# Performance work log

Measured on AMD Instinct MI355X. Metric: run time of the kernel, lower is better.

Reference implementation:

```python
import jax, jax.numpy as jnp
import numpy as np

B, IN, H = 8192, 1024, 1024


def setup_inputs() -> dict:
    key = jax.random.key(0)
    ks = jax.random.split(key, 12)
    s_in = 1.0 / np.sqrt(IN + H)  # torch Linear default init scale
    inp = {
        "x": jax.random.normal(ks[0], (B, IN), jnp.float32),
        "h_prev": jax.random.normal(ks[1], (B, H), jnp.float32),
        "c_prev": jax.random.normal(ks[2], (B, H), jnp.float32),
        "embed": jax.random.normal(ks[3], (B, H), jnp.float32),
    }
    for i, g in enumerate(("forget", "input", "update", "out")):
        inp[f"W_{g}"] = jax.random.uniform(ks[4 + 2 * i], (IN + H, H), jnp.float32, -s_in, s_in)
        inp[f"b_{g}"] = jax.random.uniform(ks[5 + 2 * i], (H,), jnp.float32, -s_in, s_in)
    return inp


def reference(x, h_prev, c_prev, embed,
              W_forget, b_forget, W_input, b_input,
              W_update, b_update, W_out, b_out):
    # cat_input: [B, IN+H]; embed is accepted but unused (matches source forward)
    cat_input = jnp.concatenate((x.reshape(x.shape[0], -1), h_prev), axis=1)
    # Fuse the 4 gate GEMMs into one [B, IN+H] x [IN+H, 4H] matmul (same math)
    W = jnp.concatenate((W_forget, W_input, W_update, W_out), axis=1)  # [IN+H, 4H]
    b = jnp.concatenate((b_forget, b_input, b_update, b_out))          # [4H]
    gates = cat_input @ W + b                                          # [B, 4H]
    f_t, i_t, g_t, o_t = jnp.split(gates, 4, axis=1)
    f_t = jax.nn.sigmoid(f_t)
    i_t = jax.nn.sigmoid(i_t)
    c_opt = jnp.tanh(g_t)
    c_t = c_prev * f_t + i_t * c_opt
    o_t = jax.nn.sigmoid(o_t)
    h_t = o_t * jnp.tanh(c_t)
    return (h_t, c_t)
```

## Files before the change

kernel.cpp:

```cpp
#include <hip/hip_runtime.h>
#include <hip/hip_bf16.h>


typedef __attribute__((ext_vector_type(8))) short short8;
typedef __attribute__((ext_vector_type(4))) float f32x4;

#define GLOBAL_AS __attribute__((address_space(1)))
#define LDS_AS    __attribute__((address_space(3)))

__device__ __forceinline__ void load_lds16(const void* g, void* l) {
  __builtin_amdgcn_global_load_lds((const GLOBAL_AS unsigned int*)g,
                                   (LDS_AS unsigned int*)l, 16, 0, 0);
}

__device__ __forceinline__ unsigned short f2bf(float f) {
  unsigned int u = __float_as_uint(f);
  unsigned int r = (u + 0x7FFFu + ((u >> 16) & 1u)) >> 16;
  return (unsigned short)r;
}

__device__ __forceinline__ float sigf(float x) {
  return 1.0f / (1.0f + __expf(-x));
}
__device__ __forceinline__ float tanh_fast(float x) {
  return 1.0f - 2.0f / (__expf(2.0f * x) + 1.0f);
}

__global__ void pack_a_kernel(const float* __restrict__ x,
                              const float* __restrict__ h,
                              unsigned short* __restrict__ Apk) {
  int t = blockIdx.x * 256 + threadIdx.x;
  int row = t >> 8;
  int c   = t & 255;
  int k   = c << 3;
  const float* src = (k < 1024) ? (x + (size_t)row * 1024 + k)
                                : (h + (size_t)row * 1024 + (k - 1024));
  float4 f0 = ((const float4*)src)[0];
  float4 f1 = ((const float4*)src)[1];
  union { unsigned short us[8]; uint4 v; } u;
  u.us[0] = f2bf(f0.x); u.us[1] = f2bf(f0.y);
  u.us[2] = f2bf(f0.z); u.us[3] = f2bf(f0.w);
  u.us[4] = f2bf(f1.x); u.us[5] = f2bf(f1.y);
  u.us[6] = f2bf(f1.z); u.us[7] = f2bf(f1.w);
  int dc = (c & ~7) | ((c & 7) ^ (row & 7));
  *(uint4*)(Apk + (size_t)row * 2048 + dc * 8) = u.v;
}

__global__ void pack_w_kernel(const float* __restrict__ W0,
                              const float* __restrict__ W1,
                              const float* __restrict__ W2,
                              const float* __restrict__ W3,
                              unsigned short* __restrict__ Wp) {
  int b  = blockIdx.x;
  int c  = b & 255;
  int nb = (b >> 8) & 3;
  int g  = b >> 10;
  const float* Wg = (g == 0) ? W0 : (g == 1) ? W1 : (g == 2) ? W2 : W3;
  int np = nb * 256 + threadIdx.x;
  int kbase = c << 3;
  union { unsigned short us[8]; uint4 v; } u;
#pragma unroll
  for (int j = 0; j < 8; ++j)
    u.us[j] = f2bf(Wg[(size_t)(kbase + j) * 1024 + np]);
  int n = (g << 10) + np;
  int dc = (c & ~7) | ((c & 7) ^ (n & 7));
  *(uint4*)(Wp + (size_t)n * 2048 + dc * 8) = u.v;
}

__global__ __launch_bounds__(256) void lstm_gemm_kernel(
    const unsigned short* __restrict__ Apk,
    const unsigned short* __restrict__ Wp,
    const float* __restrict__ c_prev,
    const float* __restrict__ bF, const float* __restrict__ bI,
    const float* __restrict__ bU, const float* __restrict__ bO,
    float* __restrict__ outH, float* __restrict__ outC) {
  __shared__ __align__(16) unsigned short Abuf[128 * 64];
  __shared__ __align__(16) unsigned short Bbuf[128 * 64];

  const int tid = threadIdx.x;
  const int l   = tid & 63;
  const int w   = tid >> 6;
  const int wr  = w >> 1;
  const int wc  = w & 1;

  int bid = blockIdx.x;
  int wg  = ((bid & 7) << 8) | (bid >> 3);
  int mblk = wg >> 5;
  int nblk = wg & 31;
  int brow  = mblk << 7;
  int ncol0 = nblk << 5;

  f32x4 acc[4][4];
#pragma unroll
  for (int g = 0; g < 4; ++g)
#pragma unroll
    for (int m = 0; m < 4; ++m) acc[g][m] = (f32x4)0.0f;

  const int seg0  = w << 2;
  const int rlane = l >> 3;
  const int clane = l & 7;

  const unsigned short* agbase =
      Apk + (size_t)(brow + seg0 * 8 + rlane) * 2048 + clane * 8;

  for (int kt = 0; kt < 32; ++kt) {
    const int kofs = kt << 6;
#pragma unroll
    for (int i = 0; i < 4; ++i) {
      load_lds16(agbase + (size_t)i * 8 * 2048 + kofs, &Abuf[(seg0 + i) * 512]);
    }
#pragma unroll
    for (int i = 0; i < 4; ++i) {
      int j = (seg0 + i) * 8 + rlane;
      int grow = ((j >> 5) << 10) + ncol0 + (j & 31);
      load_lds16(Wp + (size_t)grow * 2048 + kofs + clane * 8,
                 &Bbuf[(seg0 + i) * 512]);
    }
    __syncthreads();

#pragma unroll
    for (int kk = 0; kk < 2; ++kk) {
      const int ck = (kk << 2) | (l >> 4);
      const int sc = ck ^ (l & 7);
      short8 a[4], bfr[4];
#pragma unroll
      for (int m = 0; m < 4; ++m) {
        int row = wr * 64 + m * 16 + (l & 15);
        a[m] = *(const short8*)&Abuf[row * 64 + sc * 8];
      }
#pragma unroll
      for (int g = 0; g < 4; ++g) {
        int j = g * 32 + wc * 16 + (l & 15);
        bfr[g] = *(const short8*)&Bbuf[j * 64 + sc * 8];
      }
#pragma unroll
      for (int g = 0; g < 4; ++g)
#pragma unroll
        for (int m = 0; m < 4; ++m)
          acc[g][m] = __builtin_amdgcn_mfma_f32_16x16x32_bf16(
              a[m], bfr[g], acc[g][m], 0, 0, 0);
    }
    __syncthreads();
  }

  const int colh = ncol0 + wc * 16 + (l & 15);
  const float biasF = bF[colh], biasI = bI[colh];
  const float biasU = bU[colh], biasO = bO[colh];
  const int rowbase = brow + wr * 64 + ((l >> 4) << 2);
#pragma unroll
  for (int m = 0; m < 4; ++m) {
#pragma unroll
    for (int r = 0; r < 4; ++r) {
      int row = rowbase + m * 16 + r;
      size_t idx = (size_t)row * 1024 + colh;
      float f  = sigf(acc[0][m][r] + biasF);
      float i_ = sigf(acc[1][m][r] + biasI);
      float g_ = tanh_fast(acc[2][m][r] + biasU);
      float o_ = sigf(acc[3][m][r] + biasO);
      float cp = c_prev[idx];
      float cn = cp * f + i_ * g_;
      outH[idx] = o_ * tanh_fast(cn);
      outC[idx] = cn;
    }
  }
}

extern "C" void kernel_launch(void* const* d_in, const int* in_sizes, int n_in,
                              void* d_out, int out_size, void* d_ws, size_t ws_size,
                              hipStream_t stream) {
  const float* x      = (const float*)d_in[0];
  const float* h_prev = (const float*)d_in[1];
  const float* c_prev = (const float*)d_in[2];
  const float* Wf = (const float*)d_in[4];
  const float* bf = (const float*)d_in[5];
  const float* Wi = (const float*)d_in[6];
  const float* bi = (const float*)d_in[7];
  const float* Wu = (const float*)d_in[8];
  const float* bu = (const float*)d_in[9];
  const float* Wo = (const float*)d_in[10];
  const float* bo = (const float*)d_in[11];

  unsigned short* Apk = (unsigned short*)d_ws;
  unsigned short* Wp  = (unsigned short*)((char*)d_ws + (size_t)8192 * 2048 * 2);

  pack_a_kernel<<<8192, 256, 0, stream>>>(x, h_prev, Apk);
  pack_w_kernel<<<4096, 256, 0, stream>>>(Wf, Wi, Wu, Wo, Wp);

  float* outH = (float*)d_out;
  float* outC = outH + (size_t)8192 * 1024;
  lstm_gemm_kernel<<<2048, 256, 0, stream>>>(Apk, Wp, c_prev,
                                             bf, bi, bu, bo, outH, outC);
}
```

Baseline: 201.1 us.

## Rewrite LSTM GEMM as 256x256-tile, 8-wave, 4-stage pipelined LDS kernel

The GEMM kernel now uses 256x256 output tiles (64 hidden columns across 4 gates) with 8 waves per block and 128 KB of dynamic LDS. The LDS is a 4-slot ring of 32-wide K chunks prefetched with global_load_lds, and waits are manual vmcnt counts plus raw s_barrier. MFMA phases are split per half-tile and raised with s_setprio so loads overlap compute. Global swizzling is dropped from the pack kernels and moved into the per-lane load address. The aim is more reuse per LDS byte and hiding memory latency, at the cost of higher register pressure, a single-block-per-CU LDS footprint, and fragile hand-written synchronization.

```diff
diff --git a/kernel.cpp b/kernel.cpp
--- a/kernel.cpp
+++ b/kernel.cpp
@@ -15,13 +15,9 @@
 
 __device__ __forceinline__ unsigned short f2bf(float f) {
   unsigned int u = __float_as_uint(f);
-  unsigned int r = (u + 0x7FFFu + ((u >> 16) & 1u)) >> 16;
-  return (unsigned short)r;
-}
-
-__device__ __forceinline__ float sigf(float x) {
-  return 1.0f / (1.0f + __expf(-x));
-}
+  return (unsigned short)((u + 0x7FFFu + ((u >> 16) & 1u)) >> 16);
+}
+__device__ __forceinline__ float sigf(float x) { return 1.0f / (1.0f + __expf(-x)); }
 __device__ __forceinline__ float tanh_fast(float x) {
   return 1.0f - 2.0f / (__expf(2.0f * x) + 1.0f);
 }
@@ -42,8 +38,7 @@
   u.us[2] = f2bf(f0.z); u.us[3] = f2bf(f0.w);
   u.us[4] = f2bf(f1.x); u.us[5] = f2bf(f1.y);
   u.us[6] = f2bf(f1.z); u.us[7] = f2bf(f1.w);
-  int dc = (c & ~7) | ((c & 7) ^ (row & 7));
-  *(uint4*)(Apk + (size_t)row * 2048 + dc * 8) = u.v;
+  *(uint4*)(Apk + (size_t)row * 2048 + c * 8) = u.v;
 }
 
 __global__ void pack_w_kernel(const float* __restrict__ W0,
@@ -63,100 +58,134 @@
   for (int j = 0; j < 8; ++j)
     u.us[j] = f2bf(Wg[(size_t)(kbase + j) * 1024 + np]);
   int n = (g << 10) + np;
-  int dc = (c & ~7) | ((c & 7) ^ (n & 7));
-  *(uint4*)(Wp + (size_t)n * 2048 + dc * 8) = u.v;
-}
-
-__global__ __launch_bounds__(256) void lstm_gemm_kernel(
+  *(uint4*)(Wp + (size_t)n * 2048 + c * 8) = u.v;
+}
+
+#define MFMA16(va, vb, vc) __builtin_amdgcn_mfma_f32_16x16x32_bf16(va, vb, vc, 0, 0, 0)
+
+#define PHASE(J, Q, KTP, PSLOT, WAITN)                                         \
+  {                                                                            \
+    const int slotUS = (J) * 8192;                                             \
+    short8 av[4];                                                              \
+    _Pragma("unroll")                                                          \
+    for (int mm = 0; mm < 4; ++mm)                                             \
+      av[mm] = *(const short8*)&LDSu[slotUS + aRdBase + ((Q) * 4 + mm) * 512]; \
+    if ((Q) == 0) {                                                            \
+      _Pragma("unroll")                                                        \
+      for (int gg = 0; gg < 4; ++gg)                                           \
+        bv[gg] = *(const short8*)&LDSu[32768 + slotUS + bRdBase + gg * 512];   \
+    }                                                                          \
+    int ktp = (KTP); ktp = (ktp > 31) ? 31 : ktp;                              \
+    const int srcOfs = ktp * 64 + ((PSLOT) & 1) * 32;                          \
+    const int pbase = (PSLOT) * 8192;                                          \
+    if ((Q) == 0) {                                                            \
+      load_lds16(aSrc0 + srcOfs, &LDSu[pbase + wv * 512]);                     \
+      load_lds16(aSrc1 + srcOfs, &LDSu[pbase + 4096 + wv * 512]);              \
+    } else {                                                                   \
+      load_lds16(bSrc0 + srcOfs, &LDSu[32768 + pbase + wv * 512]);             \
+      load_lds16(bSrc1 + srcOfs, &LDSu[32768 + pbase + 4096 + wv * 512]);      \
+    }                                                                          \
+    asm volatile("s_barrier" ::: "memory");                                    \
+    __builtin_amdgcn_s_setprio(1);                                             \
+    _Pragma("unroll")                                                          \
+    for (int mm = 0; mm < 4; ++mm) {                                           \
+      _Pragma("unroll")                                                        \
+      for (int gg = 0; gg < 4; ++gg)                                           \
+        acc[(Q) * 4 + mm][gg] = MFMA16(av[mm], bv[gg], acc[(Q) * 4 + mm][gg]); \
+    }                                                                          \
+    __builtin_amdgcn_s_setprio(0);                                             \
+    if ((WAITN) == 8) asm volatile("s_waitcnt vmcnt(8)" ::: "memory");         \
+    if ((WAITN) == 4) asm volatile("s_waitcnt vmcnt(4)" ::: "memory");         \
+    asm volatile("s_barrier" ::: "memory");                                    \
+  }
+
+__global__ __launch_bounds__(512, 2) void lstm_gemm_kernel(
     const unsigned short* __restrict__ Apk,
     const unsigned short* __restrict__ Wp,
     const float* __restrict__ c_prev,
     const float* __restrict__ bF, const float* __restrict__ bI,
     const float* __restrict__ bU, const float* __restrict__ bO,
     float* __restrict__ outH, float* __restrict__ outC) {
-  __shared__ __align__(16) unsigned short Abuf[128 * 64];
-  __shared__ __align__(16) unsigned short Bbuf[128 * 64];
+  extern __shared__ unsigned short LDSu[];
 
   const int tid = threadIdx.x;
   const int l   = tid & 63;
-  const int w   = tid >> 6;
-  const int wr  = w >> 1;
-  const int wc  = w & 1;
+  const int wv  = tid >> 6;
+  const int wr  = wv >> 2;
+  const int wc  = wv & 3;
 
   int bid = blockIdx.x;
-  int wg  = ((bid & 7) << 8) | (bid >> 3);
-  int mblk = wg >> 5;
-  int nblk = wg & 31;
-  int brow  = mblk << 7;
-  int ncol0 = nblk << 5;
-
-  f32x4 acc[4][4];
-#pragma unroll
-  for (int g = 0; g < 4; ++g)
-#pragma unroll
-    for (int m = 0; m < 4; ++m) acc[g][m] = (f32x4)0.0f;
-
-  const int seg0  = w << 2;
-  const int rlane = l >> 3;
-  const int clane = l & 7;
-
-  const unsigned short* agbase =
-      Apk + (size_t)(brow + seg0 * 8 + rlane) * 2048 + clane * 8;
-
-  for (int kt = 0; kt < 32; ++kt) {
-    const int kofs = kt << 6;
-#pragma unroll
-    for (int i = 0; i < 4; ++i) {
-      load_lds16(agbase + (size_t)i * 8 * 2048 + kofs, &Abuf[(seg0 + i) * 512]);
-    }
-#pragma unroll
-    for (int i = 0; i < 4; ++i) {
-      int j = (seg0 + i) * 8 + rlane;
-      int grow = ((j >> 5) << 10) + ncol0 + (j & 31);
-      load_lds16(Wp + (size_t)grow * 2048 + kofs + clane * 8,
-                 &Bbuf[(seg0 + i) * 512]);
-    }
-    __syncthreads();
-
-#pragma unroll
-    for (int kk = 0; kk < 2; ++kk) {
-      const int ck = (kk << 2) | (l >> 4);
-      const int sc = ck ^ (l & 7);
-      short8 a[4], bfr[4];
-#pragma unroll
-      for (int m = 0; m < 4; ++m) {
-        int row = wr * 64 + m * 16 + (l & 15);
-        a[m] = *(const short8*)&Abuf[row * 64 + sc * 8];
-      }
-#pragma unroll
-      for (int g = 0; g < 4; ++g) {
-        int j = g * 32 + wc * 16 + (l & 15);
-        bfr[g] = *(const short8*)&Bbuf[j * 64 + sc * 8];
-      }
-#pragma unroll
-      for (int g = 0; g < 4; ++g)
-#pragma unroll
-        for (int m = 0; m < 4; ++m)
-          acc[g][m] = __builtin_amdgcn_mfma_f32_16x16x32_bf16(
-              a[m], bfr[g], acc[g][m], 0, 0, 0);
-    }
-    __syncthreads();
+  int wg  = ((bid & 7) << 6) | (bid >> 3);
+  const int mblk = wg >> 4;
+  const int nblk = wg & 15;
+  const int brow = mblk << 8;
+
+  const int rl  = l & 15;
+  const int cg  = l >> 4;
+  const int sc  = cg ^ ((rl >> 1) & 3);
+  const int aRdBase = (wr * 128 + rl) * 32 + sc * 8;
+  const int bRdBase = (wc * 64 + rl) * 32 + sc * 8;
+
+  const int srow = wv * 16 + (l >> 2);
+  const int csw  = ((l & 3) ^ ((l >> 3) & 3)) * 8;
+  const unsigned short* aSrc0 = Apk + (size_t)(brow + srow) * 2048 + csw;
+  const unsigned short* aSrc1 = aSrc0 + (size_t)128 * 2048;
+  int p0 = nblk * 256 + srow;
+  int n0 = (((p0 >> 4) & 3) << 10) | ((p0 >> 6) << 4) | (p0 & 15);
+  int p1 = p0 + 128;
+  int n1 = (((p1 >> 4) & 3) << 10) | ((p1 >> 6) << 4) | (p1 & 15);
+  const unsigned short* bSrc0 = Wp + (size_t)n0 * 2048 + csw;
+  const unsigned short* bSrc1 = Wp + (size_t)n1 * 2048 + csw;
+
+  f32x4 acc[8][4];
+#pragma unroll
+  for (int m = 0; m < 8; ++m)
+#pragma unroll
+    for (int g = 0; g < 4; ++g) acc[m][g] = (f32x4)0.0f;
+
+  load_lds16(aSrc0 + 0,  &LDSu[0 + wv * 512]);
+  load_lds16(aSrc1 + 0,  &LDSu[4096 + wv * 512]);
+  load_lds16(bSrc0 + 0,  &LDSu[32768 + wv * 512]);
+  load_lds16(bSrc1 + 0,  &LDSu[32768 + 4096 + wv * 512]);
+  load_lds16(aSrc0 + 32, &LDSu[8192 + wv * 512]);
+  load_lds16(aSrc1 + 32, &LDSu[8192 + 4096 + wv * 512]);
+  load_lds16(bSrc0 + 32, &LDSu[32768 + 8192 + wv * 512]);
+  load_lds16(bSrc1 + 32, &LDSu[32768 + 8192 + 4096 + wv * 512]);
+  load_lds16(aSrc0 + 64, &LDSu[16384 + wv * 512]);
+  load_lds16(aSrc1 + 64, &LDSu[16384 + 4096 + wv * 512]);
+  load_lds16(bSrc0 + 64, &LDSu[32768 + 16384 + wv * 512]);
+  load_lds16(bSrc1 + 64, &LDSu[32768 + 16384 + 4096 + wv * 512]);
+  asm volatile("s_waitcnt vmcnt(4)" ::: "memory");
+  asm volatile("s_barrier" ::: "memory");
+
+#pragma unroll 1
+  for (int it = 0; it < 16; ++it) {
+    const int k2 = it << 1;
+    short8 bv[4];
+    PHASE(0, 0, k2 + 1, 3, -1)
+    PHASE(0, 1, k2 + 1, 3, -1)
+    PHASE(1, 0, k2 + 2, 0, -1)
+    PHASE(1, 1, k2 + 2, 0, 8)
+    PHASE(2, 0, k2 + 2, 1, -1)
+    PHASE(2, 1, k2 + 2, 1, 8)
+    PHASE(3, 0, k2 + 3, 2, -1)
+    PHASE(3, 1, k2 + 3, 2, 4)
   }
 
-  const int colh = ncol0 + wc * 16 + (l & 15);
+  const int colh = nblk * 64 + wc * 16 + rl;
   const float biasF = bF[colh], biasI = bI[colh];
   const float biasU = bU[colh], biasO = bO[colh];
-  const int rowbase = brow + wr * 64 + ((l >> 4) << 2);
-#pragma unroll
-  for (int m = 0; m < 4; ++m) {
+  const int row0 = brow + wr * 128 + ((l >> 4) << 2);
+#pragma unroll
+  for (int m = 0; m < 8; ++m) {
 #pragma unroll
     for (int r = 0; r < 4; ++r) {
-      int row = rowbase + m * 16 + r;
+      int row = row0 + m * 16 + r;
       size_t idx = (size_t)row * 1024 + colh;
-      float f  = sigf(acc[0][m][r] + biasF);
-      float i_ = sigf(acc[1][m][r] + biasI);
-      float g_ = tanh_fast(acc[2][m][r] + biasU);
-      float o_ = sigf(acc[3][m][r] + biasO);
+      float f  = sigf(acc[m][0][r] + biasF);
+      float i_ = sigf(acc[m][1][r] + biasI);
+      float g_ = tanh_fast(acc[m][2][r] + biasU);
+      float o_ = sigf(acc[m][3][r] + biasO);
       float cp = c_prev[idx];
       float cn = cp * f + i_ * g_;
       outH[idx] = o_ * tanh_fast(cn);
@@ -186,8 +215,11 @@
   pack_a_kernel<<<8192, 256, 0, stream>>>(x, h_prev, Apk);
   pack_w_kernel<<<4096, 256, 0, stream>>>(Wf, Wi, Wu, Wo, Wp);
 
+  hipFuncSetAttribute((const void*)lstm_gemm_kernel,
+                      hipFuncAttributeMaxDynamicSharedMemorySize, 131072);
+
   float* outH = (float*)d_out;
   float* outC = outH + (size_t)8192 * 1024;
-  lstm_gemm_kernel<<<2048, 256, 0, stream>>>(Apk, Wp, c_prev,
-                                             bf, bi, bu, bo, outH, outC);
-}
+  lstm_gemm_kernel<<<512, 512, 131072, stream>>>(Apk, Wp, c_prev,
+                                                 bf, bi, bu, bo, outH, outC);
+}
```

After: 170.5 us. 1.18x faster.
